# Kernel optimization log

Measured on AMD Instinct MI355X. Metric: run time of the kernel, lower is better.

Reference implementation:

```python
import jax, jax.numpy as jnp
import numpy as np

IMAGE_SIZE = 256
SIGMA = 1.0   # soft-rasterization sharpness (pixels)
EPS = 1e-8


def _quat_to_rot(q):
    q = q / jnp.sqrt(jnp.sum(q * q) + EPS)
    w, x, y, z = q[0], q[1], q[2], q[3]
    return jnp.stack([
        jnp.stack([1 - 2 * (y * y + z * z), 2 * (x * y - w * z), 2 * (x * z + w * y)]),
        jnp.stack([2 * (x * y + w * z), 1 - 2 * (x * x + z * z), 2 * (y * z - w * x)]),
        jnp.stack([2 * (x * z - w * y), 2 * (y * z + w * x), 1 - 2 * (x * x + y * y)]),
    ])


def _render_silhouette(vertices, faces, q, t, K):
    # camera transform: v_cam = R(q) v + t   [V,3]
    R = _quat_to_rot(q)
    vc = vertices[0] @ R.T + t
    z = vc[:, 2] + EPS
    # perspective projection to pixel coords
    px_v = K[0, 0] * vc[:, 0] / z + K[0, 2]
    py_v = K[1, 1] * vc[:, 1] / z + K[1, 2]
    verts2d = jnp.stack([px_v, py_v], axis=-1)          # [V,2]
    tri = verts2d[faces[0]]                             # [F,3,2]

    e01 = tri[:, 1] - tri[:, 0]
    e02 = tri[:, 2] - tri[:, 0]
    area2 = e01[:, 0] * e02[:, 1] - e01[:, 1] * e02[:, 0]
    s = jnp.where(area2 >= 0, 1.0, -1.0)                # [F]

    # pixel centers
    ii, jj = jnp.meshgrid(jnp.arange(IMAGE_SIZE), jnp.arange(IMAGE_SIZE), indexing='ij')
    px = (jj.astype(jnp.float32) + 0.5).reshape(-1)     # [P]
    py = (ii.astype(jnp.float32) + 0.5).reshape(-1)     # [P]

    # signed distance to triangle = min over edges of normalized edge function
    d = None
    for k in range(3):
        a = tri[:, k]
        b = tri[:, (k + 1) % 3]
        ex = b[:, 0] - a[:, 0]
        ey = b[:, 1] - a[:, 1]
        inv_len = s / jnp.sqrt(ex * ex + ey * ey + EPS)  # sign folded in
        cx = -ey * inv_len
        cy = ex * inv_len
        c0 = (ey * a[:, 0] - ex * a[:, 1]) * inv_len
        c = px[:, None] * cx[None, :] + py[:, None] * cy[None, :] + c0[None, :]  # [P,F]
        d = c if d is None else jnp.minimum(d, c)

    # soft coverage: alpha = 1 - prod_F (1 - sigmoid(d/sigma))
    log_not_cov = jax.nn.log_sigmoid(-d / SIGMA)         # [P,F]
    sil = 1.0 - jnp.exp(jnp.sum(log_not_cov, axis=1))    # [P]
    return sil.reshape(IMAGE_SIZE, IMAGE_SIZE)


def setup_inputs() -> dict:
    key = jax.random.key(0)
    k1, k2, k3 = jax.random.split(key, 3)
    V, F = 1000, 1000
    vertices = jax.random.normal(k1, (1, V, 3), jnp.float32) * 0.3
    faces = jax.random.randint(k2, (1, F, 3), 0, V, jnp.int32)
    image_ref = jax.random.uniform(k3, (IMAGE_SIZE, IMAGE_SIZE), dtype=jnp.float32)
    q = jnp.array([1.0, 0.05, -0.03, 0.02], dtype=jnp.float32)
    t = jnp.array([0.0, 0.0, 2.732], dtype=jnp.float32)
    K = jnp.array([[280.0, 0.0, 128.0], [0.0, 280.0, 128.0], [0.0, 0.0, 1.0]], dtype=jnp.float32)
    return {"vertices": vertices, "faces": faces, "q": q, "t": t, "K": K, "image_ref": image_ref}


def reference(vertices, faces, q, t, K, image_ref):
    image = _render_silhouette(vertices, faces, q, t, K)   # [256,256]
    loss = jnp.mean((image - image_ref) ** 2, axis=1)      # per-row mean, [256]
    return loss
```

## Files before the change

### kernel.cpp

```cpp
#include <hip/hip_runtime.h>
#include <math.h>

#define IMG 256
#define NFACE 1000
#define NFP 1024
#define NWAVE 4
#define EPSF 1e-8f
#define LOG2E 1.44269504088896f
#define TCUT 16.0f
#define ACC_BREAK 25.0f
#define CULL_M (-(TCUT + 7.15f))

__device__ float g_soa[9][NFP];

__device__ __forceinline__ float bcast(float x, int s) {
    return __uint_as_float(__builtin_amdgcn_readlane(__float_as_uint(x), s));
}

__global__ __launch_bounds__(256) void k_coeff(const float* __restrict__ verts,
                                               const int* __restrict__ faces,
                                               const float* __restrict__ q,
                                               const float* __restrict__ t,
                                               const float* __restrict__ K,
                                               float* __restrict__ out) {
    int f = blockIdx.x * 256 + threadIdx.x;
    if (blockIdx.x == 0 && threadIdx.x < IMG) out[threadIdx.x] = 0.f;
    if (f >= NFP) return;

    float c[9];
    if (f < NFACE) {
        float qw = q[0], qx = q[1], qy = q[2], qz = q[3];
        float qn = sqrtf(qw * qw + qx * qx + qy * qy + qz * qz + EPSF);
        qw /= qn; qx /= qn; qy /= qn; qz /= qn;
        float R00 = 1.f - 2.f * (qy * qy + qz * qz);
        float R01 = 2.f * (qx * qy - qw * qz);
        float R02 = 2.f * (qx * qz + qw * qy);
        float R10 = 2.f * (qx * qy + qw * qz);
        float R11 = 1.f - 2.f * (qx * qx + qz * qz);
        float R12 = 2.f * (qy * qz - qw * qx);
        float R20 = 2.f * (qx * qz - qw * qy);
        float R21 = 2.f * (qy * qz + qw * qx);
        float R22 = 1.f - 2.f * (qx * qx + qy * qy);
        float tx = t[0], ty = t[1], tz = t[2];
        float K00 = K[0], K02 = K[2], K11 = K[4], K12 = K[5];

        float X[3], Y[3];
#pragma unroll
        for (int k = 0; k < 3; ++k) {
            int vi = faces[f * 3 + k];
            float vx = verts[vi * 3 + 0];
            float vy = verts[vi * 3 + 1];
            float vz = verts[vi * 3 + 2];
            float cx = R00 * vx + R01 * vy + R02 * vz + tx;
            float cy = R10 * vx + R11 * vy + R12 * vz + ty;
            float cz = R20 * vx + R21 * vy + R22 * vz + tz;
            float z = cz + EPSF;
            X[k] = K00 * cx / z + K02;
            Y[k] = K11 * cy / z + K12;
        }

        float e01x = X[1] - X[0], e01y = Y[1] - Y[0];
        float e02x = X[2] - X[0], e02y = Y[2] - Y[0];
        float area2 = e01x * e02y - e01y * e02x;
        float s = (area2 >= 0.f) ? LOG2E : -LOG2E;

#pragma unroll
        for (int k = 0; k < 3; ++k) {
            int k1 = (k + 1) % 3;
            float ex = X[k1] - X[k];
            float ey = Y[k1] - Y[k];
            float inv = s / sqrtf(ex * ex + ey * ey + EPSF);
            c[k * 3 + 0] = -ey * inv;
            c[k * 3 + 1] = ex * inv;
            c[k * 3 + 2] = (ey * X[k] - ex * Y[k]) * inv;
        }
    } else {
        c[0] = 0.f; c[1] = 0.f; c[2] = -1e9f;
        c[3] = 0.f; c[4] = 0.f; c[5] = -1e9f;
        c[6] = 0.f; c[7] = 0.f; c[8] = -1e9f;
    }

#pragma unroll
    for (int k = 0; k < 9; ++k) g_soa[k][f] = c[k];
}

__global__ __launch_bounds__(256) void k_main(const float* __restrict__ image_ref,
                                              float* __restrict__ out) {
    const int tid = threadIdx.x;
    const int wave = tid >> 6;
    const int lane = tid & 63;
    const int x0 = blockIdx.x * 8, y0 = blockIdx.y * 8;
    const int col = x0 + (lane & 7);
    const int row = y0 + (lane >> 3);
    const float px = col + 0.5f;
    const float py = row + 0.5f;
    const float tcx = x0 + 4.0f;
    const float tcy = y0 + 4.0f;

    __shared__ float s_acc[NWAVE][64];

    float acc = 0.f;
    const int wbase = wave * 256;
    for (int r = 0; r < 4; ++r) {
        const int f = wbase + r * 64 + lane;
        float l0 = g_soa[0][f], l1 = g_soa[1][f], l2 = g_soa[2][f];
        float l3 = g_soa[3][f], l4 = g_soa[4][f], l5 = g_soa[5][f];
        float l6 = g_soa[6][f], l7 = g_soa[7][f], l8 = g_soa[8][f];
        float m = fminf(fminf(fmaf(tcx, l0, fmaf(tcy, l1, l2)),
                              fmaf(tcx, l3, fmaf(tcy, l4, l5))),
                        fmaf(tcx, l6, fmaf(tcy, l7, l8)));
        unsigned long long msk = __ballot(m > CULL_M);
        while (msk) {
            int s = __ffsll((unsigned long long)msk) - 1;
            msk &= msk - 1;
            float a0 = bcast(l0, s), a1 = bcast(l1, s), a2 = bcast(l2, s);
            float b0 = bcast(l3, s), b1 = bcast(l4, s), b2 = bcast(l5, s);
            float c0 = bcast(l6, s), c1 = bcast(l7, s), c2 = bcast(l8, s);
            float u = fminf(fminf(fmaf(px, a0, fmaf(py, a1, a2)),
                                  fmaf(px, b0, fmaf(py, b1, b2))),
                            fmaf(px, c0, fmaf(py, c1, c2)));
            acc += fmaxf(u, 0.f);
            acc += __builtin_amdgcn_logf(1.f + __builtin_amdgcn_exp2f(-fabsf(u)));
        }
        if (__all(acc > ACC_BREAK)) break;
    }

    s_acc[wave][lane] = acc;
    __syncthreads();
    if (wave == 0) {
        float tot = s_acc[0][lane] + s_acc[1][lane] +
                    s_acc[2][lane] + s_acc[3][lane];
        float sil = 1.f - __builtin_amdgcn_exp2f(-tot);
        float d = sil - image_ref[row * IMG + col];
        float v = d * d;
        v += __shfl_xor(v, 1);
        v += __shfl_xor(v, 2);
        v += __shfl_xor(v, 4);
        if ((lane & 7) == 0) atomicAdd(&out[row], v * (1.f / 256.f));
    }
}

extern "C" void kernel_launch(void* const* d_in, const int* in_sizes, int n_in,
                              void* d_out, int out_size, void* d_ws, size_t ws_size,
                              hipStream_t stream) {
    const float* verts = (const float*)d_in[0];
    const int* faces = (const int*)d_in[1];
    const float* q = (const float*)d_in[2];
    const float* t = (const float*)d_in[3];
    const float* K = (const float*)d_in[4];
    const float* image_ref = (const float*)d_in[5];
    float* out = (float*)d_out;

    k_coeff<<<NFP / 256, 256, 0, stream>>>(verts, faces, q, t, K, out);
    k_main<<<dim3(IMG / 8, IMG / 8), 256, 0, stream>>>(image_ref, out);
}
```

Measured before the change: 21.22 us.

## Compact culled faces into shared memory and balance work across waves

Each wave culls its faces against the tile center, then uses a ballot and an atomic counter to append survivors to a shared-memory list capped at CAP entries. Faces that do not fit are processed inline with readlane broadcasts as before. After a barrier, all four waves split the compacted list round-robin, two faces per iteration, so imbalance in per-wave survivor counts no longer serialises the block. This adds LDS traffic, a block barrier and an atomic, and the early exit now happens inside the shared loop.

```diff
diff --git a/kernel.cpp b/kernel.cpp
--- a/kernel.cpp
+++ b/kernel.cpp
@@ -5,6 +5,7 @@
 #define NFACE 1000
 #define NFP 1024
 #define NWAVE 4
+#define CAP 320
 #define EPSF 1e-8f
 #define LOG2E 1.44269504088896f
 #define TCUT 16.0f
@@ -13,7 +14,7 @@
 
 __device__ float g_soa[9][NFP];
 
-__device__ __forceinline__ float bcast(float x, int s) {
+__device__ __forceinline__ float bcastf(float x, int s) {
     return __uint_as_float(__builtin_amdgcn_readlane(__float_as_uint(x), s));
 }
 
@@ -97,32 +98,79 @@
     const float tcx = x0 + 4.0f;
     const float tcy = y0 + 4.0f;
 
+    __shared__ float4 s_cf[CAP * 3];
     __shared__ float s_acc[NWAVE][64];
+    __shared__ int s_cnt;
+
+    if (tid == 0) s_cnt = 0;
+    __syncthreads();
+
+    float l[4][9];
+#pragma unroll
+    for (int r = 0; r < 4; ++r) {
+        const int f = r * 256 + wave * 64 + lane;
+#pragma unroll
+        for (int k = 0; k < 9; ++k) l[r][k] = g_soa[k][f];
+    }
 
     float acc = 0.f;
-    const int wbase = wave * 256;
+#pragma unroll
     for (int r = 0; r < 4; ++r) {
-        const int f = wbase + r * 64 + lane;
-        float l0 = g_soa[0][f], l1 = g_soa[1][f], l2 = g_soa[2][f];
-        float l3 = g_soa[3][f], l4 = g_soa[4][f], l5 = g_soa[5][f];
-        float l6 = g_soa[6][f], l7 = g_soa[7][f], l8 = g_soa[8][f];
-        float m = fminf(fminf(fmaf(tcx, l0, fmaf(tcy, l1, l2)),
-                              fmaf(tcx, l3, fmaf(tcy, l4, l5))),
-                        fmaf(tcx, l6, fmaf(tcy, l7, l8)));
-        unsigned long long msk = __ballot(m > CULL_M);
-        while (msk) {
-            int s = __ffsll((unsigned long long)msk) - 1;
-            msk &= msk - 1;
-            float a0 = bcast(l0, s), a1 = bcast(l1, s), a2 = bcast(l2, s);
-            float b0 = bcast(l3, s), b1 = bcast(l4, s), b2 = bcast(l5, s);
-            float c0 = bcast(l6, s), c1 = bcast(l7, s), c2 = bcast(l8, s);
+        float m = fminf(fminf(fmaf(tcx, l[r][0], fmaf(tcy, l[r][1], l[r][2])),
+                              fmaf(tcx, l[r][3], fmaf(tcy, l[r][4], l[r][5]))),
+                        fmaf(tcx, l[r][6], fmaf(tcy, l[r][7], l[r][8])));
+        bool hit = (m > CULL_M);
+        unsigned long long msk = __ballot(hit);
+        int n = __popcll(msk);
+        int base = 0;
+        if (lane == 0) base = atomicAdd(&s_cnt, n);
+        base = __builtin_amdgcn_readlane(base, 0);
+        int pos = base + __popcll(msk & ((1ull << lane) - 1ull));
+        if (hit && pos < CAP) {
+            s_cf[pos * 3 + 0] = make_float4(l[r][0], l[r][1], l[r][2], 0.f);
+            s_cf[pos * 3 + 1] = make_float4(l[r][3], l[r][4], l[r][5], 0.f);
+            s_cf[pos * 3 + 2] = make_float4(l[r][6], l[r][7], l[r][8], 0.f);
+        }
+        unsigned long long ovm = __ballot(hit && pos >= CAP);
+        while (ovm) {
+            int s = __ffsll((unsigned long long)ovm) - 1;
+            ovm &= ovm - 1;
+            float a0 = bcastf(l[r][0], s), a1 = bcastf(l[r][1], s), a2 = bcastf(l[r][2], s);
+            float b0 = bcastf(l[r][3], s), b1 = bcastf(l[r][4], s), b2 = bcastf(l[r][5], s);
+            float c0 = bcastf(l[r][6], s), c1 = bcastf(l[r][7], s), c2 = bcastf(l[r][8], s);
             float u = fminf(fminf(fmaf(px, a0, fmaf(py, a1, a2)),
                                   fmaf(px, b0, fmaf(py, b1, b2))),
                             fmaf(px, c0, fmaf(py, c1, c2)));
             acc += fmaxf(u, 0.f);
             acc += __builtin_amdgcn_logf(1.f + __builtin_amdgcn_exp2f(-fabsf(u)));
         }
-        if (__all(acc > ACC_BREAK)) break;
+    }
+    __syncthreads();
+    const int cnt = min(s_cnt, CAP);
+
+    int i = wave;
+    for (; i + 4 < cnt; i += 8) {
+        float4 aA = s_cf[i * 3], bA = s_cf[i * 3 + 1], cA = s_cf[i * 3 + 2];
+        int j = i + 4;
+        float4 aB = s_cf[j * 3], bB = s_cf[j * 3 + 1], cB = s_cf[j * 3 + 2];
+        float uA = fminf(fminf(fmaf(px, aA.x, fmaf(py, aA.y, aA.z)),
+                               fmaf(px, bA.x, fmaf(py, bA.y, bA.z))),
+                         fmaf(px, cA.x, fmaf(py, cA.y, cA.z)));
+        float uB = fminf(fminf(fmaf(px, aB.x, fmaf(py, aB.y, aB.z)),
+                               fmaf(px, bB.x, fmaf(py, bB.y, bB.z))),
+                         fmaf(px, cB.x, fmaf(py, cB.y, cB.z)));
+        acc += fmaxf(uA, 0.f) + fmaxf(uB, 0.f);
+        acc += __builtin_amdgcn_logf(1.f + __builtin_amdgcn_exp2f(-fabsf(uA)));
+        acc += __builtin_amdgcn_logf(1.f + __builtin_amdgcn_exp2f(-fabsf(uB)));
+        if (__all(acc > ACC_BREAK)) { i = cnt; break; }
+    }
+    if (i < cnt) {
+        float4 aA = s_cf[i * 3], bA = s_cf[i * 3 + 1], cA = s_cf[i * 3 + 2];
+        float u = fminf(fminf(fmaf(px, aA.x, fmaf(py, aA.y, aA.z)),
+                              fmaf(px, bA.x, fmaf(py, bA.y, bA.z))),
+                        fmaf(px, cA.x, fmaf(py, cA.y, cA.z)));
+        acc += fmaxf(u, 0.f);
+        acc += __builtin_amdgcn_logf(1.f + __builtin_amdgcn_exp2f(-fabsf(u)));
     }
 
     s_acc[wave][lane] = acc;
```

Measured after the change: 26.78 us. 1.26x slower.

## Compact culled faces into LDS and evaluate per-face-per-lane with tile early-out

Applied to the files above, without the earlier changes.

Replaces per-face readlane broadcast loop with a compaction step that writes surviving face coefficients into shared memory, then has lanes each process one face across 8 pixel rows, accumulating log terms as a product to avoid per-iteration log. Adds a tile-level lower bound on accumulated coverage to skip fully covered tiles entirely. Risks: product underflow/overflow in p, LDS capacity and occupancy cost, and changed culling bounds affecting accuracy.

```diff
diff --git a/kernel.cpp b/kernel.cpp
--- a/kernel.cpp
+++ b/kernel.cpp
@@ -5,17 +5,14 @@
 #define NFACE 1000
 #define NFP 1024
 #define NWAVE 4
+#define CAP 1024
 #define EPSF 1e-8f
 #define LOG2E 1.44269504088896f
 #define TCUT 16.0f
 #define ACC_BREAK 25.0f
-#define CULL_M (-(TCUT + 7.15f))
+#define RSLACK 7.15f
 
 __device__ float g_soa[9][NFP];
-
-__device__ __forceinline__ float bcast(float x, int s) {
-    return __uint_as_float(__builtin_amdgcn_readlane(__float_as_uint(x), s));
-}
 
 __global__ __launch_bounds__(256) void k_coeff(const float* __restrict__ verts,
                                                const int* __restrict__ faces,
@@ -90,46 +87,104 @@
     const int wave = tid >> 6;
     const int lane = tid & 63;
     const int x0 = blockIdx.x * 8, y0 = blockIdx.y * 8;
-    const int col = x0 + (lane & 7);
-    const int row = y0 + (lane >> 3);
-    const float px = col + 0.5f;
-    const float py = row + 0.5f;
     const float tcx = x0 + 4.0f;
     const float tcy = y0 + 4.0f;
 
+    __shared__ float4 s_cf[CAP * 3];
     __shared__ float s_acc[NWAVE][64];
-
-    float acc = 0.f;
+    __shared__ float s_S[NWAVE];
+    __shared__ int s_cnt;
+
+    if (tid == 0) s_cnt = 0;
+    __syncthreads();
+
     const int wbase = wave * 256;
+    float slb = 0.f;
     for (int r = 0; r < 4; ++r) {
         const int f = wbase + r * 64 + lane;
         float l0 = g_soa[0][f], l1 = g_soa[1][f], l2 = g_soa[2][f];
         float l3 = g_soa[3][f], l4 = g_soa[4][f], l5 = g_soa[5][f];
         float l6 = g_soa[6][f], l7 = g_soa[7][f], l8 = g_soa[8][f];
-        float m = fminf(fminf(fmaf(tcx, l0, fmaf(tcy, l1, l2)),
-                              fmaf(tcx, l3, fmaf(tcy, l4, l5))),
-                        fmaf(tcx, l6, fmaf(tcy, l7, l8)));
-        unsigned long long msk = __ballot(m > CULL_M);
-        while (msk) {
-            int s = __ffsll((unsigned long long)msk) - 1;
-            msk &= msk - 1;
-            float a0 = bcast(l0, s), a1 = bcast(l1, s), a2 = bcast(l2, s);
-            float b0 = bcast(l3, s), b1 = bcast(l4, s), b2 = bcast(l5, s);
-            float c0 = bcast(l6, s), c1 = bcast(l7, s), c2 = bcast(l8, s);
-            float u = fminf(fminf(fmaf(px, a0, fmaf(py, a1, a2)),
-                                  fmaf(px, b0, fmaf(py, b1, b2))),
-                            fmaf(px, c0, fmaf(py, c1, c2)));
-            acc += fmaxf(u, 0.f);
-            acc += __builtin_amdgcn_logf(1.f + __builtin_amdgcn_exp2f(-fabsf(u)));
-        }
-        if (__all(acc > ACC_BREAK)) break;
-    }
-
-    s_acc[wave][lane] = acc;
-    __syncthreads();
+        float c0 = fmaf(tcx, l0, fmaf(tcy, l1, l2));
+        float c1 = fmaf(tcx, l3, fmaf(tcy, l4, l5));
+        float c2 = fmaf(tcx, l6, fmaf(tcy, l7, l8));
+        float mc = fminf(fminf(c0, c1), c2);
+        slb += fmaxf(mc - RSLACK, 0.f);
+        float e0 = c0 + 3.5f * (fabsf(l0) + fabsf(l1));
+        float e1 = c1 + 3.5f * (fabsf(l3) + fabsf(l4));
+        float e2 = c2 + 3.5f * (fabsf(l6) + fabsf(l7));
+        bool hit = (fminf(fminf(e0, e1), e2) > -TCUT);
+        unsigned long long msk = __ballot(hit);
+        int n = __popcll(msk);
+        int base = 0;
+        if (lane == 0) base = atomicAdd(&s_cnt, n);
+        base = __builtin_amdgcn_readfirstlane(base);
+        int pos = base + __popcll(msk & ((1ull << lane) - 1ull));
+        if (hit) {
+            s_cf[pos * 3 + 0] = make_float4(l0, l1, l2, 0.f);
+            s_cf[pos * 3 + 1] = make_float4(l3, l4, l5, 0.f);
+            s_cf[pos * 3 + 2] = make_float4(l6, l7, l8, 0.f);
+        }
+    }
+#pragma unroll
+    for (int o = 1; o < 64; o <<= 1) slb += __shfl_xor(slb, o);
+    if (lane == 0) s_S[wave] = slb;
+    __syncthreads();
+
+    const int cnt = s_cnt;
+    const int cntp = (cnt + 31) & ~31;
+    if (tid < cntp - cnt) {
+        int ppos = cnt + tid;
+        s_cf[ppos * 3 + 0] = make_float4(0.f, 0.f, -1e9f, 0.f);
+        s_cf[ppos * 3 + 1] = make_float4(0.f, 0.f, -1e9f, 0.f);
+        s_cf[ppos * 3 + 2] = make_float4(0.f, 0.f, -1e9f, 0.f);
+    }
+    __syncthreads();
+    const float S_tile = s_S[0] + s_S[1] + s_S[2] + s_S[3];
+
+    if (S_tile <= ACC_BREAK) {
+        const int fs = lane >> 3;
+        const int ii = lane & 7;
+        const float pxc = x0 + ii + 0.5f;
+        float acc[8], p[8];
+#pragma unroll
+        for (int g = 0; g < 8; ++g) { acc[g] = 0.f; p[g] = 1.f; }
+
+        const int nj = cntp >> 3;
+        for (int j = wave; j < nj; j += 4) {
+            const int base = (j * 8 + fs) * 3;
+            float4 A = s_cf[base + 0];
+            float4 B = s_cf[base + 1];
+            float4 C = s_cf[base + 2];
+#pragma unroll
+            for (int g = 0; g < 8; ++g) {
+                float pyc = y0 + g + 0.5f;
+                float u = fminf(fminf(fmaf(pxc, A.x, fmaf(pyc, A.y, A.z)),
+                                      fmaf(pxc, B.x, fmaf(pyc, B.y, B.z))),
+                                fmaf(pxc, C.x, fmaf(pyc, C.y, C.z)));
+                acc[g] += fmaxf(u, 0.f);
+                float e = __builtin_amdgcn_exp2f(-fabsf(u));
+                p[g] = fmaf(p[g], e, p[g]);
+            }
+        }
+#pragma unroll
+        for (int g = 0; g < 8; ++g) {
+            float a = acc[g] + __builtin_amdgcn_logf(p[g]);
+            a += __shfl_xor(a, 8);
+            a += __shfl_xor(a, 16);
+            a += __shfl_xor(a, 32);
+            if (fs == g) s_acc[wave][g * 8 + ii] = a;
+        }
+    }
+    __syncthreads();
+
     if (wave == 0) {
-        float tot = s_acc[0][lane] + s_acc[1][lane] +
-                    s_acc[2][lane] + s_acc[3][lane];
+        const int col = x0 + (lane & 7);
+        const int row = y0 + (lane >> 3);
+        float tot = (S_tile > ACC_BREAK)
+                        ? 32.f
+                        : (s_acc[0][lane] + s_acc[1][lane] +
+                           s_acc[2][lane] + s_acc[3][lane]);
         float sil = 1.f - __builtin_amdgcn_exp2f(-tot);
         float d = sil - image_ref[row * IMG + col];
         float v = d * d;
```

Result: faster. 20.63 us (-2.8%).
